# Kernel optimization log

Measured on AMD Instinct MI355X. Metric: run time of the kernel, lower is better.

The kernel has to match this reference:

```python
import jax, jax.numpy as jnp
import numpy as np

N = 50000      # num nodes
E = 800000     # num edges (avg degree 16)
DIN = 128
DH = 128
DO = 128
BN_EPS = 1e-5


def setup_inputs() -> dict:
    key = jax.random.key(0)
    ks = jax.random.split(key, 16)
    def lin(k, i, o):
        kw, kb = jax.random.split(k)
        s = 1.0 / np.sqrt(i)
        return (jax.random.uniform(kw, (i, o), jnp.float32, -s, s),
                jax.random.uniform(kb, (o,), jnp.float32, -s, s))
    w0_1, b0_1 = lin(ks[0], DIN, DH)
    w0_2, b0_2 = lin(ks[1], DH, DH)
    w1_1, b1_1 = lin(ks[2], DH, DH)
    w1_2, b1_2 = lin(ks[3], DH, DH)
    w2_1, b2_1 = lin(ks[4], DH, DH)
    w2_2, b2_2 = lin(ks[5], DH, DO)
    return {
        "x": jax.random.normal(ks[6], (N, DIN), jnp.float32),
        "edge_index": jax.random.randint(ks[7], (2, E), 0, N, jnp.int64),
        "eps": jnp.zeros((1,), jnp.float32),
        "w0_1": w0_1, "b0_1": b0_1,
        "bn0_g": jnp.ones((DH,), jnp.float32), "bn0_b": jnp.zeros((DH,), jnp.float32),
        "w0_2": w0_2, "b0_2": b0_2,
        "n0_g": jnp.ones((DH,), jnp.float32), "n0_b": jnp.zeros((DH,), jnp.float32),
        "w1_1": w1_1, "b1_1": b1_1, "w1_2": w1_2, "b1_2": b1_2,
        "n1_g": jnp.ones((DH,), jnp.float32), "n1_b": jnp.zeros((DH,), jnp.float32),
        "w2_1": w2_1, "b2_1": b2_1, "w2_2": w2_2, "b2_2": b2_2,
        "n2_g": jnp.ones((DO,), jnp.float32), "n2_b": jnp.zeros((DO,), jnp.float32),
    }


def _bn(h, g, b):
    # BatchNorm1d in training mode: biased batch statistics over nodes
    m = h.mean(0)
    v = jnp.var(h, axis=0)
    return (h - m) * jax.lax.rsqrt(v + BN_EPS) * g + b


def reference(x, edge_index, eps, w0_1, b0_1, bn0_g, bn0_b, w0_2, b0_2, n0_g, n0_b,
              w1_1, b1_1, w1_2, b1_2, n1_g, n1_b,
              w2_1, b2_1, w2_2, b2_2, n2_g, n2_b):
    src, dst = edge_index[0], edge_index[1]

    def agg(h):
        # GIN aggregation: (1+eps)*x_i + sum_{j in N(i)} x_j
        msg = jax.ops.segment_sum(h[src], dst, num_segments=N)
        return (1.0 + eps) * h + msg

    # Layer 0: MLP = Linear -> BN -> ReLU -> Linear, then outer BN + ReLU
    h = agg(x)
    h = h @ w0_1 + b0_1
    h = jax.nn.relu(_bn(h, bn0_g, bn0_b))
    h = h @ w0_2 + b0_2
    h = jax.nn.relu(_bn(h, n0_g, n0_b))

    # Layer 1: MLP = Linear -> ReLU -> Linear, then BN + ReLU
    h = agg(h)
    h = jax.nn.relu(h @ w1_1 + b1_1)
    h = h @ w1_2 + b1_2
    h = jax.nn.relu(_bn(h, n1_g, n1_b))

    # Layer 2: MLP = Linear -> ReLU -> Linear(dim_o), then BN + ReLU
    h = agg(h)
    h = jax.nn.relu(h @ w2_1 + b2_1)
    h = h @ w2_2 + b2_2
    h = jax.nn.relu(_bn(h, n2_g, n2_b))
    return h
```

## Files before the change

kernel.cpp:

```cpp
#include <hip/hip_runtime.h>


typedef __bf16 bf16x8_t __attribute__((ext_vector_type(8)));
typedef float f32x4_t __attribute__((ext_vector_type(4)));
typedef unsigned short u16x8_t __attribute__((ext_vector_type(8)));
typedef unsigned short u16x4_t __attribute__((ext_vector_type(4)));

__device__ __forceinline__ unsigned short f2bf(float f) {
  unsigned u = __builtin_bit_cast(unsigned, f);
  u += 0x7FFFu + ((u >> 16) & 1u);
  return (unsigned short)(u >> 16);
}
__device__ __forceinline__ float bf2f(unsigned short h) {
  unsigned u = ((unsigned)h) << 16;
  return __builtin_bit_cast(float, u);
}

__global__ __launch_bounds__(256) void k_bcount(const int* __restrict__ dst,
                                                unsigned* __restrict__ tot,
                                                int E, int nb) {
  __shared__ unsigned c[256];
  c[threadIdx.x] = 0;
  __syncthreads();
  for (int e = blockIdx.x * 256 + threadIdx.x; e < E; e += gridDim.x * 256)
    atomicAdd(&c[dst[e] >> 8], 1u);
  __syncthreads();
  int t = threadIdx.x;
  if (t < nb && c[t]) atomicAdd(&tot[t], c[t]);
}

__global__ void k_bscan(const unsigned* __restrict__ tot, unsigned* __restrict__ base,
                        unsigned* __restrict__ fill, float* __restrict__ stats, int nb) {
  __shared__ unsigned s[256];
  int t = threadIdx.x;
  for (int i = t; i < 1024; i += 256) stats[i] = 0.f;
  s[t] = (t < nb) ? tot[t] : 0u;
  __syncthreads();
  for (int o = 1; o < 256; o <<= 1) {
    unsigned u = (t >= o) ? s[t - o] : 0u;
    __syncthreads();
    s[t] += u;
    __syncthreads();
  }
  unsigned excl = t ? s[t - 1] : 0u;
  if (t < nb) {
    base[t] = excl;
    fill[t] = excl;
  }
  if (t == nb) base[t] = s[nb - 1];
}

__global__ __launch_bounds__(256) void k_bucket(const int* __restrict__ src,
                                                const int* __restrict__ dst,
                                                unsigned* __restrict__ bucket_fill,
                                                unsigned* __restrict__ ebuf,
                                                int E, int nb, int chunk) {
  __shared__ unsigned cntl[256];
  __shared__ unsigned basel[256];
  __shared__ unsigned fill2[256];
  const int t = threadIdx.x;
  cntl[t] = 0;
  fill2[t] = 0;
  __syncthreads();
  const int lo = blockIdx.x * chunk;
  const int hi = (lo + chunk < E) ? lo + chunk : E;
  for (int e = lo + t; e < hi; e += 256)
    atomicAdd(&cntl[dst[e] >> 8], 1u);
  __syncthreads();
  if (t < nb) basel[t] = atomicAdd(&bucket_fill[t], cntl[t]);
  __syncthreads();
  for (int e = lo + t; e < hi; e += 256) {
    int d = dst[e];
    int b = d >> 8;
    unsigned slot = atomicAdd(&fill2[b], 1u);
    ebuf[basel[b] + slot] = ((unsigned)(d & 255) << 24) | (unsigned)src[e];
  }
}

__global__ __launch_bounds__(256) void k_build(const unsigned* __restrict__ ebuf,
                                               const unsigned* __restrict__ bucket_base,
                                               unsigned* __restrict__ csr_off,
                                               int* __restrict__ csr, int N) {
  __shared__ unsigned cntl[256];
  __shared__ unsigned scl[256];
  __shared__ unsigned startl[256];
  __shared__ unsigned filll[256];
  const int b = blockIdx.x;
  const int t = threadIdx.x;
  const unsigned ebeg = bucket_base[b];
  const unsigned eend = bucket_base[b + 1];
  cntl[t] = 0;
  filll[t] = 0;
  __syncthreads();
  for (unsigned e = ebeg + t; e < eend; e += 256)
    atomicAdd(&cntl[ebuf[e] >> 24], 1u);
  __syncthreads();
  unsigned v = cntl[t];
  scl[t] = v;
  __syncthreads();
  for (int o = 1; o < 256; o <<= 1) {
    unsigned u = (t >= o) ? scl[t - o] : 0u;
    __syncthreads();
    scl[t] += u;
    __syncthreads();
  }
  int node = b * 256 + t;
  if (node < N) csr_off[node] = ebeg + scl[t];
  startl[t] = scl[t] - v;
  __syncthreads();
  for (unsigned e = ebeg + t; e < eend; e += 256) {
    unsigned p = ebuf[e];
    unsigned d = p >> 24;
    unsigned slot = atomicAdd(&filll[d], 1u);
    csr[ebeg + startl[d] + slot] = (int)(p & 0xFFFFFFu);
  }
}

__global__ void k_wtx(const float* w0, const float* w1, const float* w2,
                      const float* w3, const float* w4, const float* w5,
                      unsigned short* __restrict__ wT,
                      const float* __restrict__ x, unsigned short* __restrict__ xb,
                      int total8) {
  if (blockIdx.x < 96) {
    const float* ws[6] = {w0, w1, w2, w3, w4, w5};
    int m = blockIdx.x >> 4;
    int tl = blockIdx.x & 15;
    int tr = (tl >> 2) * 32;
    int tc = (tl & 3) * 32;
    const float* W = ws[m];
    __shared__ float sm[32][33];
    int r = threadIdx.x >> 3;
    int c4 = (threadIdx.x & 7) * 4;
    float4 v = *reinterpret_cast<const float4*>(&W[(tr + r) * 128 + tc + c4]);
    sm[r][c4 + 0] = v.x; sm[r][c4 + 1] = v.y; sm[r][c4 + 2] = v.z; sm[r][c4 + 3] = v.w;
    __syncthreads();
    u16x4_t o;
    o[0] = f2bf(sm[c4 + 0][r]);
    o[1] = f2bf(sm[c4 + 1][r]);
    o[2] = f2bf(sm[c4 + 2][r]);
    o[3] = f2bf(sm[c4 + 3][r]);
    *reinterpret_cast<u16x4_t*>(&wT[(size_t)m * 16384 + (tc + r) * 128 + tr + c4]) = o;
  } else {
    int i = (blockIdx.x - 96) * 256 + threadIdx.x;
    if (i >= total8) return;
    const float* p = x + (size_t)i * 8;
    float4 f0 = *reinterpret_cast<const float4*>(p);
    float4 f1 = *reinterpret_cast<const float4*>(p + 4);
    u16x8_t o;
    o[0] = f2bf(f0.x); o[1] = f2bf(f0.y); o[2] = f2bf(f0.z); o[3] = f2bf(f0.w);
    o[4] = f2bf(f1.x); o[5] = f2bf(f1.y); o[6] = f2bf(f1.z); o[7] = f2bf(f1.w);
    *reinterpret_cast<u16x8_t*>(xb + (size_t)i * 8) = o;
  }
}

template<int MODE>
__global__ __launch_bounds__(256) void k_agg(
    const unsigned short* __restrict__ Zv, const float* __restrict__ Zself,
    const float* __restrict__ ssum, const float* __restrict__ ssq,
    const float* __restrict__ gg, const float* __restrict__ bb,
    const int* __restrict__ csr, const unsigned* __restrict__ offend,
    const float* __restrict__ epsp, unsigned short* __restrict__ out, int N) {
  __shared__ float scl[128], shl[128];
  const int tid = threadIdx.x;
  if (MODE == 1) {
    if (tid < 128) {
      float inv = 1.f / (float)N;
      float m = ssum[tid] * inv;
      float vv = ssq[tid] * inv - m * m;
      float s = gg[tid] * rsqrtf(vv + 1e-5f);
      scl[tid] = s;
      shl[tid] = bb[tid] - m * s;
    }
    __syncthreads();
  }
  int node = blockIdx.x * 4 + (tid >> 6);
  if (node >= N) return;
  const int lane = tid & 63;
  const int sub = lane >> 4;
  const int t = lane & 15;
  const int c0 = t * 8;

  float sc[8], sh[8];
  if (MODE == 1) {
#pragma unroll
    for (int j = 0; j < 8; ++j) { sc[j] = scl[c0 + j]; sh[j] = shl[c0 + j]; }
  }

  float s[8];
#pragma unroll
  for (int j = 0; j < 8; ++j) s[j] = 0.f;

  auto accum = [&](int row) {
    u16x8_t v = *reinterpret_cast<const u16x8_t*>(Zv + (size_t)row * 128 + c0);
    if (MODE == 0) {
#pragma unroll
      for (int j = 0; j < 8; ++j) s[j] += bf2f(v[j]);
    } else {
#pragma unroll
      for (int j = 0; j < 8; ++j) s[j] += fmaxf(bf2f(v[j]) * sc[j] + sh[j], 0.f);
    }
  };

  const unsigned beg = node ? offend[node - 1] : 0u;
  const unsigned end = offend[node];
  const int deg = (int)(end - beg);
  const int deg64 = deg < 64 ? deg : 64;

  int idx = (lane < deg64) ? csr[beg + lane] : 0;

  const int nIter = (deg64 + 3) >> 2;
  int p = sub;
  int i = 0;
  for (; i + 4 <= nIter; i += 4, p += 16) {
    int r0 = __shfl(idx, p);
    int r1 = __shfl(idx, p + 4);
    int r2 = __shfl(idx, p + 8);
    int r3 = __shfl(idx, p + 12);
    if (p < deg64) accum(r0);
    if (p + 4 < deg64) accum(r1);
    if (p + 8 < deg64) accum(r2);
    if (p + 12 < deg64) accum(r3);
  }
  for (; i < nIter; ++i, p += 4) {
    int r0 = __shfl(idx, p);
    if (p < deg64) accum(r0);
  }

  for (int e = 64 + sub; e < deg; e += 4) accum(csr[beg + e]);

  if (sub == 0) {
    float ep = 1.f + epsp[0];
    if (MODE == 0) {
      const float* Z = Zself + (size_t)node * 128 + c0;
      float4 f0 = *reinterpret_cast<const float4*>(Z);
      float4 f1 = *reinterpret_cast<const float4*>(Z + 4);
      s[0] += ep * f0.x; s[1] += ep * f0.y; s[2] += ep * f0.z; s[3] += ep * f0.w;
      s[4] += ep * f1.x; s[5] += ep * f1.y; s[6] += ep * f1.z; s[7] += ep * f1.w;
    } else {
      u16x8_t v = *reinterpret_cast<const u16x8_t*>(Zv + (size_t)node * 128 + c0);
#pragma unroll
      for (int j = 0; j < 8; ++j)
        s[j] += ep * fmaxf(bf2f(v[j]) * sc[j] + sh[j], 0.f);
    }
  }

#pragma unroll
  for (int j = 0; j < 8; ++j) {
    s[j] += __shfl_xor(s[j], 16);
    s[j] += __shfl_xor(s[j], 32);
  }

  if (sub == 0) {
    u16x8_t o;
#pragma unroll
    for (int j = 0; j < 8; ++j) o[j] = f2bf(s[j]);
    *reinterpret_cast<u16x8_t*>(out + (size_t)node * 128 + c0) = o;
  }
}

template<bool IN_BN, bool OUT_RELU, bool STATS>
__global__ __launch_bounds__(256) void k_mm(
    const unsigned short* __restrict__ A,
    const float* __restrict__ ssum, const float* __restrict__ ssq,
    const float* __restrict__ gg, const float* __restrict__ bb,
    const unsigned short* __restrict__ BT, const float* __restrict__ bias,
    unsigned short* __restrict__ Y, float* __restrict__ osum, float* __restrict__ osq,
    int M, int N) {
  __shared__ __attribute__((aligned(16))) unsigned short Bl[128][136];
  __shared__ float cs[128], cq[128];
  __shared__ float scl[128], shl[128];
  const int tid = threadIdx.x;
  const int r0 = blockIdx.x * 128;
  const int trow = tid >> 4;
  const int tch = (tid & 15) * 8;

#pragma unroll
  for (int pass = 0; pass < 8; ++pass) {
    int n = pass * 16 + trow;
    u16x8_t v = *reinterpret_cast<const u16x8_t*>(&BT[(size_t)n * 128 + tch]);
    *reinterpret_cast<u16x8_t*>(&Bl[n][tch]) = v;
  }
  if (IN_BN && tid < 128) {
    float inv = 1.f / (float)N;
    float m = ssum[tid] * inv;
    float vv = ssq[tid] * inv - m * m;
    float s = gg[tid] * rsqrtf(vv + 1e-5f);
    scl[tid] = s;
    shl[tid] = bb[tid] - m * s;
  }
  if (STATS && tid < 128) { cs[tid] = 0.f; cq[tid] = 0.f; }

  const int wave = tid >> 6;
  const int lane = tid & 63;
  const int lr = lane & 15;
  const int lkb = (lane >> 4) * 8;
  const int wr = r0 + wave * 32;

  u16x8_t araw[2][4];
  const u16x8_t zv = {0, 0, 0, 0, 0, 0, 0, 0};
#pragma unroll
  for (int mr = 0; mr < 2; ++mr) {
    int grow = wr + mr * 16 + lr;
    bool ok = grow < M;
    const unsigned short* Ar = A + (size_t)grow * 128 + lkb;
#pragma unroll
    for (int kc = 0; kc < 4; ++kc)
      araw[mr][kc] = ok ? *reinterpret_cast<const u16x8_t*>(Ar + kc * 32) : zv;
  }
  __syncthreads();

  if (IN_BN) {
#pragma unroll
    for (int kc = 0; kc < 4; ++kc) {
      float scv[8], shv[8];
#pragma unroll
      for (int j = 0; j < 8; ++j) {
        int c = kc * 32 + lkb + j;
        scv[j] = scl[c]; shv[j] = shl[c];
      }
#pragma unroll
      for (int mr = 0; mr < 2; ++mr) {
#pragma unroll
        for (int j = 0; j < 8; ++j)
          araw[mr][kc][j] = f2bf(fmaxf(bf2f(araw[mr][kc][j]) * scv[j] + shv[j], 0.f));
      }
    }
  }

  f32x4_t acc[2][8];
  f32x4_t zero = {0.f, 0.f, 0.f, 0.f};
#pragma unroll
  for (int mr = 0; mr < 2; ++mr)
#pragma unroll
    for (int i = 0; i < 8; ++i) acc[mr][i] = zero;

#pragma unroll
  for (int kc = 0; kc < 4; ++kc) {
    bf16x8_t a0 = __builtin_bit_cast(bf16x8_t, araw[0][kc]);
    bf16x8_t a1 = __builtin_bit_cast(bf16x8_t, araw[1][kc]);
#pragma unroll
    for (int nt = 0; nt < 8; ++nt) {
      bf16x8_t bf = __builtin_bit_cast(bf16x8_t,
          *reinterpret_cast<const u16x8_t*>(&Bl[nt * 16 + lr][kc * 32 + lkb]));
      acc[0][nt] = __builtin_amdgcn_mfma_f32_16x16x32_bf16(a0, bf, acc[0][nt], 0, 0, 0);
      acc[1][nt] = __builtin_amdgcn_mfma_f32_16x16x32_bf16(a1, bf, acc[1][nt], 0, 0, 0);
    }
  }

  const int g = lane >> 4;
#pragma unroll
  for (int mr = 0; mr < 2; ++mr) {
#pragma unroll
    for (int nt = 0; nt < 8; ++nt) {
      int col = nt * 16 + lr;
      float bv = bias[col];
      float s4 = 0.f, q4 = 0.f;
#pragma unroll
      for (int j = 0; j < 4; ++j) {
        int gr = wr + mr * 16 + g * 4 + j;
        float v = acc[mr][nt][j] + bv;
        if (OUT_RELU) v = fmaxf(v, 0.f);
        if (gr < M) {
          Y[(size_t)gr * 128 + col] = f2bf(v);
          if (STATS) { s4 += v; q4 += v * v; }
        }
      }
      if (STATS) {
        s4 += __shfl_xor(s4, 16);
        s4 += __shfl_xor(s4, 32);
        q4 += __shfl_xor(q4, 16);
        q4 += __shfl_xor(q4, 32);
        if (lane < 16) { atomicAdd(&cs[col], s4); atomicAdd(&cq[col], q4); }
      }
    }
  }
  if (STATS) {
    __syncthreads();
    if (tid < 128) {
      atomicAdd(&osum[tid], cs[tid]);
      atomicAdd(&osq[tid], cq[tid]);
    }
  }
}

__global__ __launch_bounds__(256) void k_mm2x(
    const unsigned short* __restrict__ A,
    const unsigned short* __restrict__ BT1, const float* __restrict__ bias1,
    const unsigned short* __restrict__ BT2, const float* __restrict__ bias2,
    unsigned short* __restrict__ Y, float* __restrict__ osum, float* __restrict__ osq,
    int M) {
  __shared__ __attribute__((aligned(16))) unsigned short Al[128][136];
  __shared__ __attribute__((aligned(16))) unsigned short Bl[128][136];
  __shared__ float cs[128], cq[128];
  const int tid = threadIdx.x;
  const int r0 = blockIdx.x * 128;
  const int trow = tid >> 4;
  const int tch = (tid & 15) * 8;

#pragma unroll
  for (int pass = 0; pass < 8; ++pass) {
    int n = pass * 16 + trow;
    u16x8_t v = *reinterpret_cast<const u16x8_t*>(&BT1[(size_t)n * 128 + tch]);
    *reinterpret_cast<u16x8_t*>(&Bl[n][tch]) = v;
  }
  if (tid < 128) { cs[tid] = 0.f; cq[tid] = 0.f; }

  const int wave = tid >> 6;
  const int lane = tid & 63;
  const int lr = lane & 15;
  const int lkb = (lane >> 4) * 8;
  const int wr = r0 + wave * 32;
  const int g = lane >> 4;

  u16x8_t araw[2][4];
  const u16x8_t zv = {0, 0, 0, 0, 0, 0, 0, 0};
#pragma unroll
  for (int mr = 0; mr < 2; ++mr) {
    int grow = wr + mr * 16 + lr;
    bool ok = grow < M;
    const unsigned short* Ar = A + (size_t)grow * 128 + lkb;
#pragma unroll
    for (int kc = 0; kc < 4; ++kc)
      araw[mr][kc] = ok ? *reinterpret_cast<const u16x8_t*>(Ar + kc * 32) : zv;
  }
  __syncthreads();

  f32x4_t acc[2][8];
  f32x4_t zero = {0.f, 0.f, 0.f, 0.f};
#pragma unroll
  for (int mr = 0; mr < 2; ++mr)
#pragma unroll
    for (int i = 0; i < 8; ++i) acc[mr][i] = zero;

#pragma unroll
  for (int kc = 0; kc < 4; ++kc) {
    bf16x8_t a0 = __builtin_bit_cast(bf16x8_t, araw[0][kc]);
    bf16x8_t a1 = __builtin_bit_cast(bf16x8_t, araw[1][kc]);
#pragma unroll
    for (int nt = 0; nt < 8; ++nt) {
      bf16x8_t bf = __builtin_bit_cast(bf16x8_t,
          *reinterpret_cast<const u16x8_t*>(&Bl[nt * 16 + lr][kc * 32 + lkb]));
      acc[0][nt] = __builtin_amdgcn_mfma_f32_16x16x32_bf16(a0, bf, acc[0][nt], 0, 0, 0);
      acc[1][nt] = __builtin_amdgcn_mfma_f32_16x16x32_bf16(a1, bf, acc[1][nt], 0, 0, 0);
    }
  }
  __syncthreads();

#pragma unroll
  for (int pass = 0; pass < 8; ++pass) {
    int n = pass * 16 + trow;
    u16x8_t v = *reinterpret_cast<const u16x8_t*>(&BT2[(size_t)n * 128 + tch]);
    *reinterpret_cast<u16x8_t*>(&Bl[n][tch]) = v;
  }
#pragma unroll
  for (int mr = 0; mr < 2; ++mr) {
#pragma unroll
    for (int nt = 0; nt < 8; ++nt) {
      int col = nt * 16 + lr;
      float bv = bias1[col];
#pragma unroll
      for (int j = 0; j < 4; ++j) {
        Al[wave * 32 + mr * 16 + g * 4 + j][col] = f2bf(fmaxf(acc[mr][nt][j] + bv, 0.f));
      }
    }
  }
  __syncthreads();

#pragma unroll
  for (int mr = 0; mr < 2; ++mr)
#pragma unroll
    for (int i = 0; i < 8; ++i) acc[mr][i] = zero;
#pragma unroll
  for (int kc = 0; kc < 4; ++kc) {
    bf16x8_t a0 = __builtin_bit_cast(bf16x8_t,
        *reinterpret_cast<const u16x8_t*>(&Al[wave * 32 + lr][kc * 32 + lkb]));
    bf16x8_t a1 = __builtin_bit_cast(bf16x8_t,
        *reinterpret_cast<const u16x8_t*>(&Al[wave * 32 + 16 + lr][kc * 32 + lkb]));
#pragma unroll
    for (int nt = 0; nt < 8; ++nt) {
      bf16x8_t bf = __builtin_bit_cast(bf16x8_t,
          *reinterpret_cast<const u16x8_t*>(&Bl[nt * 16 + lr][kc * 32 + lkb]));
      acc[0][nt] = __builtin_amdgcn_mfma_f32_16x16x32_bf16(a0, bf, acc[0][nt], 0, 0, 0);
      acc[1][nt] = __builtin_amdgcn_mfma_f32_16x16x32_bf16(a1, bf, acc[1][nt], 0, 0, 0);
    }
  }

#pragma unroll
  for (int mr = 0; mr < 2; ++mr) {
#pragma unroll
    for (int nt = 0; nt < 8; ++nt) {
      int col = nt * 16 + lr;
      float bv = bias2[col];
      float s4 = 0.f, q4 = 0.f;
#pragma unroll
      for (int j = 0; j < 4; ++j) {
        int gr = wr + mr * 16 + g * 4 + j;
        float v = acc[mr][nt][j] + bv;
        if (gr < M) {
          Y[(size_t)gr * 128 + col] = f2bf(v);
          s4 += v; q4 += v * v;
        }
      }
      s4 += __shfl_xor(s4, 16);
      s4 += __shfl_xor(s4, 32);
      q4 += __shfl_xor(q4, 16);
      q4 += __shfl_xor(q4, 32);
      if (lane < 16) { atomicAdd(&cs[col], s4); atomicAdd(&cq[col], q4); }
    }
  }
  __syncthreads();
  if (tid < 128) {
    atomicAdd(&osum[tid], cs[tid]);
    atomicAdd(&osq[tid], cq[tid]);
  }
}

__global__ void k_final(const unsigned short* __restrict__ Y,
                        const float* __restrict__ ssum, const float* __restrict__ ssq,
                        const float* __restrict__ gg, const float* __restrict__ bb,
                        float* __restrict__ out, int total8, int N) {
  __shared__ float scl[128], shl[128];
  const int tid = threadIdx.x;
  if (tid < 128) {
    float inv = 1.f / (float)N;
    float m = ssum[tid] * inv;
    float vv = ssq[tid] * inv - m * m;
    float s = gg[tid] * rsqrtf(vv + 1e-5f);
    scl[tid] = s;
    shl[tid] = bb[tid] - m * s;
  }
  __syncthreads();
  int i = blockIdx.x * 256 + tid;
  if (i >= total8) return;
  int base = i * 8;
  int c = base & 127;
  u16x8_t v = *reinterpret_cast<const u16x8_t*>(&Y[base]);
  float4 o0, o1;
  o0.x = fmaxf(bf2f(v[0]) * scl[c + 0] + shl[c + 0], 0.f);
  o0.y = fmaxf(bf2f(v[1]) * scl[c + 1] + shl[c + 1], 0.f);
  o0.z = fmaxf(bf2f(v[2]) * scl[c + 2] + shl[c + 2], 0.f);
  o0.w = fmaxf(bf2f(v[3]) * scl[c + 3] + shl[c + 3], 0.f);
  o1.x = fmaxf(bf2f(v[4]) * scl[c + 4] + shl[c + 4], 0.f);
  o1.y = fmaxf(bf2f(v[5]) * scl[c + 5] + shl[c + 5], 0.f);
  o1.z = fmaxf(bf2f(v[6]) * scl[c + 6] + shl[c + 6], 0.f);
  o1.w = fmaxf(bf2f(v[7]) * scl[c + 7] + shl[c + 7], 0.f);
  *reinterpret_cast<float4*>(&out[base]) = o0;
  *reinterpret_cast<float4*>(&out[base + 4]) = o1;
}

extern "C" void kernel_launch(void* const* d_in, const int* in_sizes, int n_in,
                              void* d_out, int out_size, void* d_ws, size_t ws_size,
                              hipStream_t stream) {
  (void)n_in; (void)out_size; (void)ws_size;
  const float* x = (const float*)d_in[0];
  const int* ei = (const int*)d_in[1];
  const float* eps = (const float*)d_in[2];
  const int N = in_sizes[0] / 128;
  const int E = in_sizes[1] / 2;
  const int* src = ei;
  const int* dst = ei + E;

  char* ws = (char*)d_ws;
  size_t off = 0;
  auto alloc = [&](size_t bytes) -> char* {
    char* p = ws + off;
    off += (bytes + 255) & ~(size_t)255;
    return p;
  };
  unsigned* csr_off = (unsigned*)alloc((size_t)N * 4);
  int* csr_src = (int*)alloc((size_t)E * 4);
  unsigned* bucket_tot = (unsigned*)alloc(256 * 4);
  unsigned* bucket_base = (unsigned*)alloc(257 * 4);
  unsigned* bucket_fill = (unsigned*)alloc(256 * 4);
  float* stats = (float*)alloc(8 * 128 * 4);
  unsigned short* wT = (unsigned short*)alloc(6 * 128 * 128 * 2);
  unsigned short* xb = (unsigned short*)alloc((size_t)N * 128 * 2);
  unsigned short* B1 = (unsigned short*)alloc((size_t)N * 128 * 2);
  unsigned short* B2 = (unsigned short*)alloc((size_t)N * 128 * 2);
  unsigned* ebuf = (unsigned*)B1;

  hipMemsetAsync(bucket_tot, 0, 256 * 4, stream);

  const int NBUCK = (N + 255) >> 8;
  const int gA = (N + 3) / 4;
  const int gM = (N + 127) / 128;
  const int gF = ((N * 128 / 8) + 255) / 256;
  const int chunk = (E + 255) / 256;

  k_bcount<<<256, 256, 0, stream>>>(dst, bucket_tot, E, NBUCK);
  k_bscan<<<1, 256, 0, stream>>>(bucket_tot, bucket_base, bucket_fill, stats, NBUCK);
  k_bucket<<<256, 256, 0, stream>>>(src, dst, bucket_fill, ebuf, E, NBUCK, chunk);
  k_build<<<NBUCK, 256, 0, stream>>>(ebuf, bucket_base, csr_off, csr_src, N);
  k_wtx<<<96 + gF, 256, 0, stream>>>((const float*)d_in[3], (const float*)d_in[7],
                                     (const float*)d_in[11], (const float*)d_in[13],
                                     (const float*)d_in[17], (const float*)d_in[19], wT,
                                     x, xb, N * 128 / 8);

  k_agg<0><<<gA, 256, 0, stream>>>(xb, x, nullptr, nullptr, nullptr, nullptr,
                                   csr_src, csr_off, eps, B1, N);
  k_mm<false, false, true><<<gM, 256, 0, stream>>>(B1, nullptr, nullptr, nullptr, nullptr,
      wT + 0 * 16384, (const float*)d_in[4], B2, stats + 0, stats + 128, N, N);
  k_mm<true, false, true><<<gM, 256, 0, stream>>>(B2, stats + 0, stats + 128,
      (const float*)d_in[5], (const float*)d_in[6],
      wT + 1 * 16384, (const float*)d_in[8], B1, stats + 256, stats + 384, N, N);

  k_agg<1><<<gA, 256, 0, stream>>>(B1, nullptr, stats + 256, stats + 384,
                                   (const float*)d_in[9], (const float*)d_in[10],
                                   csr_src, csr_off, eps, B2, N);
  k_mm2x<<<gM, 256, 0, stream>>>(B2, wT + 2 * 16384, (const float*)d_in[12],
      wT + 3 * 16384, (const float*)d_in[14], B1, stats + 512, stats + 640, N);

  k_agg<1><<<gA, 256, 0, stream>>>(B1, nullptr, stats + 512, stats + 640,
                                   (const float*)d_in[15], (const float*)d_in[16],
                                   csr_src, csr_off, eps, B2, N);
  k_mm2x<<<gM, 256, 0, stream>>>(B2, wT + 4 * 16384, (const float*)d_in[18],
      wT + 5 * 16384, (const float*)d_in[20], B1, stats + 768, stats + 896, N);

  k_final<<<gF, 256, 0, stream>>>(B1, stats + 768, stats + 896,
                                  (const float*)d_in[21], (const float*)d_in[22],
                                  (float*)d_out, N * 128 / 8, N);
}
```

Before: 270.7 us.

## Fuse GIN neighbor aggregation into the following MFMA matmul kernels

Each layer's gather-sum aggregation is merged into the matmul kernel. A 512-thread block aggregates its 128 node rows straight into shared memory and then runs the MFMA GEMM (or the pair of GEMMs) on that tile, so the aggregated tensor never makes a round trip through global memory and three kernel launches go away. In exchange, the gather phase now runs with 8 waves per block processing 16 rows each sequentially, giving less latency-hiding parallelism than the old 4-nodes-per-block launch. The block also waits at a barrier before the GEMM, and k_mm is specialised to always apply the input BN.

```diff
diff --git a/kernel.cpp b/kernel.cpp
--- a/kernel.cpp
+++ b/kernel.cpp
@@ -153,112 +153,218 @@
   }
 }
 
-template<int MODE>
-__global__ __launch_bounds__(256) void k_agg(
+template<int MODE, bool PAIR>
+__global__ __launch_bounds__(512, 4) void k_fused(
     const unsigned short* __restrict__ Zv, const float* __restrict__ Zself,
     const float* __restrict__ ssum, const float* __restrict__ ssq,
     const float* __restrict__ gg, const float* __restrict__ bb,
     const int* __restrict__ csr, const unsigned* __restrict__ offend,
-    const float* __restrict__ epsp, unsigned short* __restrict__ out, int N) {
+    const float* __restrict__ epsp,
+    const unsigned short* __restrict__ BT1, const float* __restrict__ bias1,
+    const unsigned short* __restrict__ BT2, const float* __restrict__ bias2,
+    unsigned short* __restrict__ Y, float* __restrict__ osum, float* __restrict__ osq,
+    int M, int N) {
+  __shared__ __attribute__((aligned(16))) unsigned short Al[128][136];
+  __shared__ __attribute__((aligned(16))) unsigned short Bl[128][136];
+  __shared__ float cs[128], cq[128];
   __shared__ float scl[128], shl[128];
   const int tid = threadIdx.x;
-  if (MODE == 1) {
-    if (tid < 128) {
-      float inv = 1.f / (float)N;
-      float m = ssum[tid] * inv;
-      float vv = ssq[tid] * inv - m * m;
-      float s = gg[tid] * rsqrtf(vv + 1e-5f);
-      scl[tid] = s;
-      shl[tid] = bb[tid] - m * s;
-    }
-    __syncthreads();
-  }
-  int node = blockIdx.x * 4 + (tid >> 6);
-  if (node >= N) return;
+  const int r0 = blockIdx.x * 128;
+  const int trow = tid >> 4;
+  const int tch = (tid & 15) * 8;
+
+#pragma unroll
+  for (int pass = 0; pass < 4; ++pass) {
+    int n = pass * 32 + trow;
+    *reinterpret_cast<u16x8_t*>(&Bl[n][tch]) =
+        *reinterpret_cast<const u16x8_t*>(&BT1[(size_t)n * 128 + tch]);
+  }
+  if (MODE == 1 && tid < 128) {
+    float inv = 1.f / (float)N;
+    float m = ssum[tid] * inv;
+    float vv = ssq[tid] * inv - m * m;
+    float s = gg[tid] * rsqrtf(vv + 1e-5f);
+    scl[tid] = s;
+    shl[tid] = bb[tid] - m * s;
+  }
+  if (tid < 128) { cs[tid] = 0.f; cq[tid] = 0.f; }
+  if (MODE == 1) __syncthreads();
+
+  const int wave = tid >> 6;
   const int lane = tid & 63;
   const int sub = lane >> 4;
-  const int t = lane & 15;
-  const int c0 = t * 8;
+  const int lr = lane & 15;
+  const int c0 = lr * 8;
+  const int lkb = sub * 8;
 
   float sc[8], sh[8];
   if (MODE == 1) {
 #pragma unroll
     for (int j = 0; j < 8; ++j) { sc[j] = scl[c0 + j]; sh[j] = shl[c0 + j]; }
   }
-
-  float s[8];
-#pragma unroll
-  for (int j = 0; j < 8; ++j) s[j] = 0.f;
-
-  auto accum = [&](int row) {
-    u16x8_t v = *reinterpret_cast<const u16x8_t*>(Zv + (size_t)row * 128 + c0);
-    if (MODE == 0) {
-#pragma unroll
-      for (int j = 0; j < 8; ++j) s[j] += bf2f(v[j]);
-    } else {
-#pragma unroll
-      for (int j = 0; j < 8; ++j) s[j] += fmaxf(bf2f(v[j]) * sc[j] + sh[j], 0.f);
-    }
-  };
-
-  const unsigned beg = node ? offend[node - 1] : 0u;
-  const unsigned end = offend[node];
-  const int deg = (int)(end - beg);
-  const int deg64 = deg < 64 ? deg : 64;
-
-  int idx = (lane < deg64) ? csr[beg + lane] : 0;
-
-  const int nIter = (deg64 + 3) >> 2;
-  int p = sub;
-  int i = 0;
-  for (; i + 4 <= nIter; i += 4, p += 16) {
-    int r0 = __shfl(idx, p);
-    int r1 = __shfl(idx, p + 4);
-    int r2 = __shfl(idx, p + 8);
-    int r3 = __shfl(idx, p + 12);
-    if (p < deg64) accum(r0);
-    if (p + 4 < deg64) accum(r1);
-    if (p + 8 < deg64) accum(r2);
-    if (p + 12 < deg64) accum(r3);
-  }
-  for (; i < nIter; ++i, p += 4) {
-    int r0 = __shfl(idx, p);
-    if (p < deg64) accum(r0);
-  }
-
-  for (int e = 64 + sub; e < deg; e += 4) accum(csr[beg + e]);
-
-  if (sub == 0) {
-    float ep = 1.f + epsp[0];
-    if (MODE == 0) {
-      const float* Z = Zself + (size_t)node * 128 + c0;
-      float4 f0 = *reinterpret_cast<const float4*>(Z);
-      float4 f1 = *reinterpret_cast<const float4*>(Z + 4);
-      s[0] += ep * f0.x; s[1] += ep * f0.y; s[2] += ep * f0.z; s[3] += ep * f0.w;
-      s[4] += ep * f1.x; s[5] += ep * f1.y; s[6] += ep * f1.z; s[7] += ep * f1.w;
-    } else {
-      u16x8_t v = *reinterpret_cast<const u16x8_t*>(Zv + (size_t)node * 128 + c0);
-#pragma unroll
-      for (int j = 0; j < 8; ++j)
-        s[j] += ep * fmaxf(bf2f(v[j]) * sc[j] + sh[j], 0.f);
-    }
-  }
-
-#pragma unroll
-  for (int j = 0; j < 8; ++j) {
-    s[j] += __shfl_xor(s[j], 16);
-    s[j] += __shfl_xor(s[j], 32);
-  }
-
-  if (sub == 0) {
-    u16x8_t o;
-#pragma unroll
-    for (int j = 0; j < 8; ++j) o[j] = f2bf(s[j]);
-    *reinterpret_cast<u16x8_t*>(out + (size_t)node * 128 + c0) = o;
-  }
-}
-
-template<bool IN_BN, bool OUT_RELU, bool STATS>
+  const float ep = 1.f + epsp[0];
+
+  for (int i16 = 0; i16 < 16; ++i16) {
+    const int row = wave * 16 + i16;
+    const int node = r0 + row;
+    if (node >= N) break;
+
+    float s[8];
+#pragma unroll
+    for (int j = 0; j < 8; ++j) s[j] = 0.f;
+
+    auto accum = [&](int rw) {
+      u16x8_t v = *reinterpret_cast<const u16x8_t*>(Zv + (size_t)rw * 128 + c0);
+      if (MODE == 0) {
+#pragma unroll
+        for (int j = 0; j < 8; ++j) s[j] += bf2f(v[j]);
+      } else {
+#pragma unroll
+        for (int j = 0; j < 8; ++j) s[j] += fmaxf(bf2f(v[j]) * sc[j] + sh[j], 0.f);
+      }
+    };
+
+    const unsigned beg = node ? offend[node - 1] : 0u;
+    const unsigned end = offend[node];
+    const int deg = (int)(end - beg);
+    const int deg64 = deg < 64 ? deg : 64;
+
+    int idx = (lane < deg64) ? csr[beg + lane] : 0;
+
+    const int nIter = (deg64 + 3) >> 2;
+    int p = sub;
+    int i = 0;
+    for (; i + 4 <= nIter; i += 4, p += 16) {
+      int rw0 = __shfl(idx, p);
+      int rw1 = __shfl(idx, p + 4);
+      int rw2 = __shfl(idx, p + 8);
+      int rw3 = __shfl(idx, p + 12);
+      if (p < deg64) accum(rw0);
+      if (p + 4 < deg64) accum(rw1);
+      if (p + 8 < deg64) accum(rw2);
+      if (p + 12 < deg64) accum(rw3);
+    }
+    for (; i < nIter; ++i, p += 4) {
+      int rw0 = __shfl(idx, p);
+      if (p < deg64) accum(rw0);
+    }
+    for (int e = 64 + sub; e < deg; e += 4) accum(csr[beg + e]);
+
+    if (sub == 0) {
+      if (MODE == 0) {
+        const float* Z = Zself + (size_t)node * 128 + c0;
+        float4 f0 = *reinterpret_cast<const float4*>(Z);
+        float4 f1 = *reinterpret_cast<const float4*>(Z + 4);
+        s[0] += ep * f0.x; s[1] += ep * f0.y; s[2] += ep * f0.z; s[3] += ep * f0.w;
+        s[4] += ep * f1.x; s[5] += ep * f1.y; s[6] += ep * f1.z; s[7] += ep * f1.w;
+      } else {
+        u16x8_t v = *reinterpret_cast<const u16x8_t*>(Zv + (size_t)node * 128 + c0);
+#pragma unroll
+        for (int j = 0; j < 8; ++j)
+          s[j] += ep * fmaxf(bf2f(v[j]) * sc[j] + sh[j], 0.f);
+      }
+    }
+
+#pragma unroll
+    for (int j = 0; j < 8; ++j) {
+      s[j] += __shfl_xor(s[j], 16);
+      s[j] += __shfl_xor(s[j], 32);
+    }
+
+    if (sub == 0) {
+      u16x8_t o;
+#pragma unroll
+      for (int j = 0; j < 8; ++j) o[j] = f2bf(s[j]);
+      *reinterpret_cast<u16x8_t*>(&Al[row][c0]) = o;
+    }
+  }
+  __syncthreads();
+
+  u16x8_t araw[4];
+#pragma unroll
+  for (int kc = 0; kc < 4; ++kc)
+    araw[kc] = *reinterpret_cast<const u16x8_t*>(&Al[wave * 16 + lr][kc * 32 + lkb]);
+
+  f32x4_t acc[8];
+  f32x4_t zero = {0.f, 0.f, 0.f, 0.f};
+#pragma unroll
+  for (int i = 0; i < 8; ++i) acc[i] = zero;
+
+#pragma unroll
+  for (int kc = 0; kc < 4; ++kc) {
+    bf16x8_t af = __builtin_bit_cast(bf16x8_t, araw[kc]);
+#pragma unroll
+    for (int nt = 0; nt < 8; ++nt) {
+      bf16x8_t bf = __builtin_bit_cast(bf16x8_t,
+          *reinterpret_cast<const u16x8_t*>(&Bl[nt * 16 + lr][kc * 32 + lkb]));
+      acc[nt] = __builtin_amdgcn_mfma_f32_16x16x32_bf16(af, bf, acc[nt], 0, 0, 0);
+    }
+  }
+
+  const int g = lane >> 4;
+  if (PAIR) {
+    __syncthreads();
+#pragma unroll
+    for (int pass = 0; pass < 4; ++pass) {
+      int n = pass * 32 + trow;
+      *reinterpret_cast<u16x8_t*>(&Bl[n][tch]) =
+          *reinterpret_cast<const u16x8_t*>(&BT2[(size_t)n * 128 + tch]);
+    }
+#pragma unroll
+    for (int nt = 0; nt < 8; ++nt) {
+      int col = nt * 16 + lr;
+      float bv = bias1[col];
+#pragma unroll
+      for (int j = 0; j < 4; ++j)
+        Al[wave * 16 + g * 4 + j][col] = f2bf(fmaxf(acc[nt][j] + bv, 0.f));
+    }
+    __syncthreads();
+
+#pragma unroll
+    for (int kc = 0; kc < 4; ++kc)
+      araw[kc] = *reinterpret_cast<const u16x8_t*>(&Al[wave * 16 + lr][kc * 32 + lkb]);
+#pragma unroll
+    for (int i = 0; i < 8; ++i) acc[i] = zero;
+#pragma unroll
+    for (int kc = 0; kc < 4; ++kc) {
+      bf16x8_t af = __builtin_bit_cast(bf16x8_t, araw[kc]);
+#pragma unroll
+      for (int nt = 0; nt < 8; ++nt) {
+        bf16x8_t bf = __builtin_bit_cast(bf16x8_t,
+            *reinterpret_cast<const u16x8_t*>(&Bl[nt * 16 + lr][kc * 32 + lkb]));
+        acc[nt] = __builtin_amdgcn_mfma_f32_16x16x32_bf16(af, bf, acc[nt], 0, 0, 0);
+      }
+    }
+  }
+
+  const float* bias = PAIR ? bias2 : bias1;
+#pragma unroll
+  for (int nt = 0; nt < 8; ++nt) {
+    int col = nt * 16 + lr;
+    float bv = bias[col];
+    float s4 = 0.f, q4 = 0.f;
+#pragma unroll
+    for (int j = 0; j < 4; ++j) {
+      int gr = r0 + wave * 16 + g * 4 + j;
+      float v = acc[nt][j] + bv;
+      if (gr < M) {
+        Y[(size_t)gr * 128 + col] = f2bf(v);
+        s4 += v; q4 += v * v;
+      }
+    }
+    s4 += __shfl_xor(s4, 16);
+    s4 += __shfl_xor(s4, 32);
+    q4 += __shfl_xor(q4, 16);
+    q4 += __shfl_xor(q4, 32);
+    if (lane < 16) { atomicAdd(&cs[col], s4); atomicAdd(&cq[col], q4); }
+  }
+  __syncthreads();
+  if (tid < 128) {
+    atomicAdd(&osum[tid], cs[tid]);
+    atomicAdd(&osq[tid], cq[tid]);
+  }
+}
+
 __global__ __launch_bounds__(256) void k_mm(
     const unsigned short* __restrict__ A,
     const float* __restrict__ ssum, const float* __restrict__ ssq,
@@ -280,15 +386,15 @@
     u16x8_t v = *reinterpret_cast<const u16x8_t*>(&BT[(size_t)n * 128 + tch]);
     *reinterpret_cast<u16x8_t*>(&Bl[n][tch]) = v;
   }
-  if (IN_BN && tid < 128) {
+  if (tid < 128) {
     float inv = 1.f / (float)N;
     float m = ssum[tid] * inv;
     float vv = ssq[tid] * inv - m * m;
     float s = gg[tid] * rsqrtf(vv + 1e-5f);
     scl[tid] = s;
     shl[tid] = bb[tid] - m * s;
-  }
-  if (STATS && tid < 128) { cs[tid] = 0.f; cq[tid] = 0.f; }
+    cs[tid] = 0.f; cq[tid] = 0.f;
+  }
 
   const int wave = tid >> 6;
   const int lane = tid & 63;
@@ -309,21 +415,19 @@
   }
   __syncthreads();
 
-  if (IN_BN) {
-#pragma unroll
-    for (int kc = 0; kc < 4; ++kc) {
-      float scv[8], shv[8];
-#pragma unroll
-      for (int j = 0; j < 8; ++j) {
-        int c = kc * 32 + lkb + j;
-        scv[j] = scl[c]; shv[j] = shl[c];
-      }
-#pragma unroll
-      for (int mr = 0; mr < 2; ++mr) {
-#pragma unroll
-        for (int j = 0; j < 8; ++j)
-          araw[mr][kc][j] = f2bf(fmaxf(bf2f(araw[mr][kc][j]) * scv[j] + shv[j], 0.f));
-      }
+#pragma unroll
+  for (int kc = 0; kc < 4; ++kc) {
+    float scv[8], shv[8];
+#pragma unroll
+    for (int j = 0; j < 8; ++j) {
+      int c = kc * 32 + lkb + j;
+      scv[j] = scl[c]; shv[j] = shl[c];
+    }
+#pragma unroll
+    for (int mr = 0; mr < 2; ++mr) {
+#pragma unroll
+      for (int j = 0; j < 8; ++j)
+        araw[mr][kc][j] = f2bf(fmaxf(bf2f(araw[mr][kc][j]) * scv[j] + shv[j], 0.f));
     }
   }
 
@@ -354,143 +458,6 @@
     for (int nt = 0; nt < 8; ++nt) {
       int col = nt * 16 + lr;
       float bv = bias[col];
-      float s4 = 0.f, q4 = 0.f;
-#pragma unroll
-      for (int j = 0; j < 4; ++j) {
-        int gr = wr + mr * 16 + g * 4 + j;
-        float v = acc[mr][nt][j] + bv;
-        if (OUT_RELU) v = fmaxf(v, 0.f);
-        if (gr < M) {
-          Y[(size_t)gr * 128 + col] = f2bf(v);
-          if (STATS) { s4 += v; q4 += v * v; }
-        }
-      }
-      if (STATS) {
-        s4 += __shfl_xor(s4, 16);
-        s4 += __shfl_xor(s4, 32);
-        q4 += __shfl_xor(q4, 16);
-        q4 += __shfl_xor(q4, 32);
-        if (lane < 16) { atomicAdd(&cs[col], s4); atomicAdd(&cq[col], q4); }
-      }
-    }
-  }
-  if (STATS) {
-    __syncthreads();
-    if (tid < 128) {
-      atomicAdd(&osum[tid], cs[tid]);
-      atomicAdd(&osq[tid], cq[tid]);
-    }
-  }
-}
-
-__global__ __launch_bounds__(256) void k_mm2x(
-    const unsigned short* __restrict__ A,
-    const unsigned short* __restrict__ BT1, const float* __restrict__ bias1,
-    const unsigned short* __restrict__ BT2, const float* __restrict__ bias2,
-    unsigned short* __restrict__ Y, float* __restrict__ osum, float* __restrict__ osq,
-    int M) {
-  __shared__ __attribute__((aligned(16))) unsigned short Al[128][136];
-  __shared__ __attribute__((aligned(16))) unsigned short Bl[128][136];
-  __shared__ float cs[128], cq[128];
-  const int tid = threadIdx.x;
-  const int r0 = blockIdx.x * 128;
-  const int trow = tid >> 4;
-  const int tch = (tid & 15) * 8;
-
-#pragma unroll
-  for (int pass = 0; pass < 8; ++pass) {
-    int n = pass * 16 + trow;
-    u16x8_t v = *reinterpret_cast<const u16x8_t*>(&BT1[(size_t)n * 128 + tch]);
-    *reinterpret_cast<u16x8_t*>(&Bl[n][tch]) = v;
-  }
-  if (tid < 128) { cs[tid] = 0.f; cq[tid] = 0.f; }
-
-  const int wave = tid >> 6;
-  const int lane = tid & 63;
-  const int lr = lane & 15;
-  const int lkb = (lane >> 4) * 8;
-  const int wr = r0 + wave * 32;
-  const int g = lane >> 4;
-
-  u16x8_t araw[2][4];
-  const u16x8_t zv = {0, 0, 0, 0, 0, 0, 0, 0};
-#pragma unroll
-  for (int mr = 0; mr < 2; ++mr) {
-    int grow = wr + mr * 16 + lr;
-    bool ok = grow < M;
-    const unsigned short* Ar = A + (size_t)grow * 128 + lkb;
-#pragma unroll
-    for (int kc = 0; kc < 4; ++kc)
-      araw[mr][kc] = ok ? *reinterpret_cast<const u16x8_t*>(Ar + kc * 32) : zv;
-  }
-  __syncthreads();
-
-  f32x4_t acc[2][8];
-  f32x4_t zero = {0.f, 0.f, 0.f, 0.f};
-#pragma unroll
-  for (int mr = 0; mr < 2; ++mr)
-#pragma unroll
-    for (int i = 0; i < 8; ++i) acc[mr][i] = zero;
-
-#pragma unroll
-  for (int kc = 0; kc < 4; ++kc) {
-    bf16x8_t a0 = __builtin_bit_cast(bf16x8_t, araw[0][kc]);
-    bf16x8_t a1 = __builtin_bit_cast(bf16x8_t, araw[1][kc]);
-#pragma unroll
-    for (int nt = 0; nt < 8; ++nt) {
-      bf16x8_t bf = __builtin_bit_cast(bf16x8_t,
-          *reinterpret_cast<const u16x8_t*>(&Bl[nt * 16 + lr][kc * 32 + lkb]));
-      acc[0][nt] = __builtin_amdgcn_mfma_f32_16x16x32_bf16(a0, bf, acc[0][nt], 0, 0, 0);
-      acc[1][nt] = __builtin_amdgcn_mfma_f32_16x16x32_bf16(a1, bf, acc[1][nt], 0, 0, 0);
-    }
-  }
-  __syncthreads();
-
-#pragma unroll
-  for (int pass = 0; pass < 8; ++pass) {
-    int n = pass * 16 + trow;
-    u16x8_t v = *reinterpret_cast<const u16x8_t*>(&BT2[(size_t)n * 128 + tch]);
-    *reinterpret_cast<u16x8_t*>(&Bl[n][tch]) = v;
-  }
-#pragma unroll
-  for (int mr = 0; mr < 2; ++mr) {
-#pragma unroll
-    for (int nt = 0; nt < 8; ++nt) {
-      int col = nt * 16 + lr;
-      float bv = bias1[col];
-#pragma unroll
-      for (int j = 0; j < 4; ++j) {
-        Al[wave * 32 + mr * 16 + g * 4 + j][col] = f2bf(fmaxf(acc[mr][nt][j] + bv, 0.f));
-      }
-    }
-  }
-  __syncthreads();
-
-#pragma unroll
-  for (int mr = 0; mr < 2; ++mr)
-#pragma unroll
-    for (int i = 0; i < 8; ++i) acc[mr][i] = zero;
-#pragma unroll
-  for (int kc = 0; kc < 4; ++kc) {
-    bf16x8_t a0 = __builtin_bit_cast(bf16x8_t,
-        *reinterpret_cast<const u16x8_t*>(&Al[wave * 32 + lr][kc * 32 + lkb]));
-    bf16x8_t a1 = __builtin_bit_cast(bf16x8_t,
-        *reinterpret_cast<const u16x8_t*>(&Al[wave * 32 + 16 + lr][kc * 32 + lkb]));
-#pragma unroll
-    for (int nt = 0; nt < 8; ++nt) {
-      bf16x8_t bf = __builtin_bit_cast(bf16x8_t,
-          *reinterpret_cast<const u16x8_t*>(&Bl[nt * 16 + lr][kc * 32 + lkb]));
-      acc[0][nt] = __builtin_amdgcn_mfma_f32_16x16x32_bf16(a0, bf, acc[0][nt], 0, 0, 0);
-      acc[1][nt] = __builtin_amdgcn_mfma_f32_16x16x32_bf16(a1, bf, acc[1][nt], 0, 0, 0);
-    }
-  }
-
-#pragma unroll
-  for (int mr = 0; mr < 2; ++mr) {
-#pragma unroll
-    for (int nt = 0; nt < 8; ++nt) {
-      int col = nt * 16 + lr;
-      float bv = bias2[col];
       float s4 = 0.f, q4 = 0.f;
 #pragma unroll
       for (int j = 0; j < 4; ++j) {
@@ -582,7 +549,6 @@
   hipMemsetAsync(bucket_tot, 0, 256 * 4, stream);
 
   const int NBUCK = (N + 255) >> 8;
-  const int gA = (N + 3) / 4;
   const int gM = (N + 127) / 128;
   const int gF = ((N * 128 / 8) + 255) / 256;
   const int chunk = (E + 255) / 256;
@@ -596,25 +562,22 @@
                                      (const float*)d_in[17], (const float*)d_in[19], wT,
                                      x, xb, N * 128 / 8);
 
-  k_agg<0><<<gA, 256, 0, stream>>>(xb, x, nullptr, nullptr, nullptr, nullptr,
-                                   csr_src, csr_off, eps, B1, N);
-  k_mm<false, false, true><<<gM, 256, 0, stream>>>(B1, nullptr, nullptr, nullptr, nullptr,
-      wT + 0 * 16384, (const float*)d_in[4], B2, stats + 0, stats + 128, N, N);
-  k_mm<true, false, true><<<gM, 256, 0, stream>>>(B2, stats + 0, stats + 128,
+  k_fused<0, false><<<gM, 512, 0, stream>>>(xb, x, nullptr, nullptr, nullptr, nullptr,
+      csr_src, csr_off, eps, wT + 0 * 16384, (const float*)d_in[4], nullptr, nullptr,
+      B2, stats + 0, stats + 128, N, N);
+  k_mm<<<gM, 256, 0, stream>>>(B2, stats + 0, stats + 128,
       (const float*)d_in[5], (const float*)d_in[6],
       wT + 1 * 16384, (const float*)d_in[8], B1, stats + 256, stats + 384, N, N);
 
-  k_agg<1><<<gA, 256, 0, stream>>>(B1, nullptr, stats + 256, stats + 384,
-                                   (const float*)d_in[9], (const float*)d_in[10],
-                                   csr_src, csr_off, eps, B2, N);
-  k_mm2x<<<gM, 256, 0, stream>>>(B2, wT + 2 * 16384, (const float*)d_in[12],
-      wT + 3 * 16384, (const float*)d_in[14], B1, stats + 512, stats + 640, N);
-
-  k_agg<1><<<gA, 256, 0, stream>>>(B1, nullptr, stats + 512, stats + 640,
-                                   (const float*)d_in[15], (const float*)d_in[16],
-                                   csr_src, csr_off, eps, B2, N);
-  k_mm2x<<<gM, 256, 0, stream>>>(B2, wT + 4 * 16384, (const float*)d_in[18],
-      wT + 5 * 16384, (const float*)d_in[20], B1, stats + 768, stats + 896, N);
+  k_fused<1, true><<<gM, 512, 0, stream>>>(B1, nullptr, stats + 256, stats + 384,
+      (const float*)d_in[9], (const float*)d_in[10],
+      csr_src, csr_off, eps, wT + 2 * 16384, (const float*)d_in[12],
+      wT + 3 * 16384, (const float*)d_in[14], B2, stats + 512, stats + 640, N, N);
+
+  k_fused<1, true><<<gM, 512, 0, stream>>>(B2, nullptr, stats + 512, stats + 640,
+      (const float*)d_in[15], (const float*)d_in[16],
+      csr_src, csr_off, eps, wT + 4 * 16384, (const float*)d_in[18],
+      wT + 5 * 16384, (const float*)d_in[20], B1, stats + 768, stats + 896, N, N);
 
   k_final<<<gF, 256, 0, stream>>>(B1, stats + 768, stats + 896,
                                   (const float*)d_in[21], (const float*)d_in[22],
```

Result: slower. 301.1 us (+11.2%).
